# Kernel optimization log

Hardware: AMD Instinct MI355X
Metric: run time of the kernel (lower is better)

Reference implementation:

```python
import jax, jax.numpy as jnp
import numpy as np

B = 8
S = 512  # seq_len


def setup_inputs() -> dict:
    key = jax.random.key(0)
    kx, kw, kb = jax.random.split(key, 3)
    x = jax.random.normal(kx, (B, S, S), dtype=jnp.float32)
    # Padded block of per-diagonal Linear weights: W[i, k, j] is weight[k, j]
    # of nn.Linear(i+1, i+1); entries with k > i or j > i are zero.
    i_d = jnp.arange(S)[:, None, None]
    k_d = jnp.arange(S)[None, :, None]
    j_d = jnp.arange(S)[None, None, :]
    wmask = ((k_d <= i_d) & (j_d <= i_d)).astype(jnp.float32)
    W = jax.random.normal(kw, (S, S, S), dtype=jnp.float32) * 0.02 * wmask
    bmask = (jnp.arange(S)[None, :] <= jnp.arange(S)[:, None]).astype(jnp.float32)
    b = jax.random.normal(kb, (S, S), dtype=jnp.float32) * 0.02 * bmask
    return {"x": x, "W": W, "b": b}


def reference(x, W, b):
    # For each anti-diagonal i (positions (r, i-r), r=0..i, with r+c=i<S):
    #   gather d = x[:, r, i-r], apply Linear_i: out = d @ W_i^T + b_i,
    #   scatter back reversed: x[:, r, i-r] = out[i-r]  =>  x[b,r,c]=out[b,r+c,c].
    S_ = x.shape[-1]
    i_idx = jnp.arange(S_)[:, None]   # diagonal index
    r_idx = jnp.arange(S_)[None, :]   # position along diagonal
    cols = (i_idx - r_idx) % S_
    valid = (r_idx <= i_idx)[None]                       # [1,S,S]
    # D[b, i, r] = x[b, r, i-r] for r<=i else 0
    D = jnp.where(valid, x[:, r_idx, cols], 0.0)         # [B,S,S]
    # Batched per-diagonal matmul: out[b,i,k] = sum_j W[i,k,j] D[b,i,j] + b[i,k]
    out = jnp.einsum('bij,ikj->bik', D, W) + b[None]     # [B,S,S]
    # Scatter back with reversal: x[b,r,c] = out[b, r+c, c] when r+c < S
    rr = jnp.arange(S_)[:, None]
    cc = jnp.arange(S_)[None, :]
    diag = rr + cc
    ok = (diag < S_)[None]
    new_x = jnp.where(ok, out[:, jnp.minimum(diag, S_ - 1), cc], x)
    return new_x
```

## Files before the change

kernel.cpp:

```cpp
#include <hip/hip_runtime.h>

#define S 512
#define NB 8
#define KT 256
#define JT 32

__global__ __launch_bounds__(256) void tail_copy_kernel(const float* __restrict__ x,
                                                        float* __restrict__ out) {
  int idx = blockIdx.x * 256 + threadIdx.x;
  int c = idx & (S - 1);
  int r = (idx >> 9) & (S - 1);
  if (r + c >= S) out[idx] = x[idx];
}

__global__ __launch_bounds__(256, 3) void diag_linear_kernel(const float* __restrict__ x,
                                                             const float* __restrict__ W,
                                                             const float* __restrict__ bias,
                                                             float* __restrict__ out) {
  __shared__ __align__(16) float WtBuf[JT * KT];
  __shared__ __align__(16) float DlBuf[S * NB];

  const int bx = (int)blockIdx.x;
  const int u  = bx >> 3;
  const int xc = bx & 7;
  const int i  = (S - 1) - ((u & 15) + 16 * (xc + 8 * (u >> 4)));
  const int k0 = (int)blockIdx.y * KT;
  if (k0 > i) return;

  const int tid  = threadIdx.x;
  const int wave = tid >> 6;
  const int lane = tid & 63;

  const int jend = (i + JT) & ~(JT - 1);
  const int T    = jend >> 5;

  for (int idx = tid; idx < jend * NB; idx += 256) {
    const int j = idx >> 3;
    const int b = idx & 7;
    DlBuf[idx] = (j <= i) ? x[b * (S * S) + j * S + (i - j)] : 0.0f;
  }

  float acc[4][NB];
#pragma unroll
  for (int m = 0; m < 4; ++m)
#pragma unroll
    for (int b = 0; b < NB; ++b) acc[m][b] = 0.0f;

  const int  k       = k0 + tid;
  const bool krow_ok = (k <= i);
  const float* wrow  = W + ((size_t)i * S + k) * S;

  float4 v[2][8];
  if (!krow_ok) {
#pragma unroll
    for (int g = 0; g < 2; ++g)
#pragma unroll
      for (int q = 0; q < 8; ++q) v[g][q] = make_float4(0.f, 0.f, 0.f, 0.f);
  }

#define LOAD_GRP(g, J0)                                                        \
  if (krow_ok) {                                                               \
    _Pragma("unroll")                                                          \
    for (int q = 0; q < 8; ++q)                                                \
      v[g][q] = *(const float4*)(wrow + (J0) + 4 * q);                         \
  }

  LOAD_GRP(0, 0)
  if (T > 1) LOAD_GRP(1, 32)

  for (int t = 0; t < T; ++t) {
    const int pb = t & 1;
    const int j0 = t << 5;
    __syncthreads();
    {
      const float4* vv = v[pb];
#pragma unroll
      for (int q = 0; q < 8; ++q) {
        WtBuf[(4 * q + 0) * KT + tid] = vv[q].x;
        WtBuf[(4 * q + 1) * KT + tid] = vv[q].y;
        WtBuf[(4 * q + 2) * KT + tid] = vv[q].z;
        WtBuf[(4 * q + 3) * KT + tid] = vv[q].w;
      }
    }
    const int tn = t + 2;
    if (tn < T) LOAD_GRP(pb, tn << 5)
    __syncthreads();

#pragma unroll
    for (int uu = 0; uu < 8; ++uu) {
      const int jl = (wave << 3) + uu;
      const float4 wv = *(const float4*)&WtBuf[jl * KT + (lane << 2)];
      const float4 dA = *(const float4*)&DlBuf[(j0 + jl) * NB];
      const float4 dB = *(const float4*)&DlBuf[(j0 + jl) * NB + 4];
      const float wm[4] = {wv.x, wv.y, wv.z, wv.w};
#pragma unroll
      for (int m = 0; m < 4; ++m) {
        acc[m][0] = fmaf(wm[m], dA.x, acc[m][0]);
        acc[m][1] = fmaf(wm[m], dA.y, acc[m][1]);
        acc[m][2] = fmaf(wm[m], dA.z, acc[m][2]);
        acc[m][3] = fmaf(wm[m], dA.w, acc[m][3]);
        acc[m][4] = fmaf(wm[m], dB.x, acc[m][4]);
        acc[m][5] = fmaf(wm[m], dB.y, acc[m][5]);
        acc[m][6] = fmaf(wm[m], dB.z, acc[m][6]);
        acc[m][7] = fmaf(wm[m], dB.w, acc[m][7]);
      }
    }
  }

  __syncthreads();
  float* Racc = WtBuf;

  for (int w = 0; w < 4; ++w) {
    if (wave == w) {
#pragma unroll
      for (int b = 0; b < NB; ++b) {
        float4* p = (float4*)&Racc[b * KT + (lane << 2)];
        float4 cur = make_float4(acc[0][b], acc[1][b], acc[2][b], acc[3][b]);
        if (w != 0) {
          float4 old = *p;
          cur.x += old.x; cur.y += old.y; cur.z += old.z; cur.w += old.w;
        }
        *p = cur;
      }
    }
    __syncthreads();
  }

  if (krow_ok) {
    const float bv = bias[i * S + k];
    const int r = i - k;
#pragma unroll
    for (int b = 0; b < NB; ++b)
      out[b * (S * S) + r * S + k] = Racc[b * KT + tid] + bv;
  }
}

extern "C" void kernel_launch(void* const* d_in, const int* in_sizes, int n_in,
                              void* d_out, int out_size, void* d_ws, size_t ws_size,
                              hipStream_t stream) {
  const float* x    = (const float*)d_in[0];
  const float* W    = (const float*)d_in[1];
  const float* bias = (const float*)d_in[2];
  float* out = (float*)d_out;

  (void)d_ws; (void)ws_size; (void)in_sizes; (void)n_in; (void)out_size;

  tail_copy_kernel<<<dim3((NB * S * S) / 256), 256, 0, stream>>>(x, out);
  diag_linear_kernel<<<dim3(S, 2), 256, 0, stream>>>(x, W, bias, out);
}
```

Baseline: 716.9 us.

## Halve k-tile to 128 rows and split j-columns across thread halves

Cuts each block's k-tile from 256 to 128 rows, so the grid grows from 2 to 4 tiles in y. Within a block, the two halves of the threads each load a different 16-column slice of the W row. Each thread now keeps 2 accumulator rows instead of 4, which lowers register pressure and lets the occupancy hint rise to 4 blocks. The intent is more blocks and better load balance across the triangular workload, which matters because this kernel is bandwidth bound on W. The custom block-to-diagonal swizzle is replaced with a plain linear mapping. The cost is that the D gather is repeated by more blocks.

```diff
diff --git a/kernel.cpp b/kernel.cpp
--- a/kernel.cpp
+++ b/kernel.cpp
@@ -2,7 +2,7 @@
 
 #define S 512
 #define NB 8
-#define KT 256
+#define KT 128
 #define JT 32
 
 __global__ __launch_bounds__(256) void tail_copy_kernel(const float* __restrict__ x,
@@ -13,17 +13,14 @@
   if (r + c >= S) out[idx] = x[idx];
 }
 
-__global__ __launch_bounds__(256, 3) void diag_linear_kernel(const float* __restrict__ x,
+__global__ __launch_bounds__(256, 4) void diag_linear_kernel(const float* __restrict__ x,
                                                              const float* __restrict__ W,
                                                              const float* __restrict__ bias,
                                                              float* __restrict__ out) {
   __shared__ __align__(16) float WtBuf[JT * KT];
   __shared__ __align__(16) float DlBuf[S * NB];
 
-  const int bx = (int)blockIdx.x;
-  const int u  = bx >> 3;
-  const int xc = bx & 7;
-  const int i  = (S - 1) - ((u & 15) + 16 * (xc + 8 * (u >> 4)));
+  const int i  = (S - 1) - (int)blockIdx.x;
   const int k0 = (int)blockIdx.y * KT;
   if (k0 > i) return;
 
@@ -40,28 +37,30 @@
     DlBuf[idx] = (j <= i) ? x[b * (S * S) + j * S + (i - j)] : 0.0f;
   }
 
-  float acc[4][NB];
+  const int kl_r = tid & (KT - 1);
+  const int h    = tid >> 7;
+  const int  k_r     = k0 + kl_r;
+  const bool krow_ok = (k_r <= i);
+  const float* wrow  = W + ((size_t)i * S + k_r) * S + (h << 4);
+
+  float acc[2][NB];
 #pragma unroll
-  for (int m = 0; m < 4; ++m)
+  for (int m = 0; m < 2; ++m)
 #pragma unroll
     for (int b = 0; b < NB; ++b) acc[m][b] = 0.0f;
 
-  const int  k       = k0 + tid;
-  const bool krow_ok = (k <= i);
-  const float* wrow  = W + ((size_t)i * S + k) * S;
-
-  float4 v[2][8];
+  float4 v[2][4];
   if (!krow_ok) {
 #pragma unroll
     for (int g = 0; g < 2; ++g)
 #pragma unroll
-      for (int q = 0; q < 8; ++q) v[g][q] = make_float4(0.f, 0.f, 0.f, 0.f);
+      for (int q = 0; q < 4; ++q) v[g][q] = make_float4(0.f, 0.f, 0.f, 0.f);
   }
 
 #define LOAD_GRP(g, J0)                                                        \
   if (krow_ok) {                                                               \
     _Pragma("unroll")                                                          \
-    for (int q = 0; q < 8; ++q)                                                \
+    for (int q = 0; q < 4; ++q)                                                \
       v[g][q] = *(const float4*)(wrow + (J0) + 4 * q);                         \
   }
 
@@ -75,11 +74,12 @@
     {
       const float4* vv = v[pb];
 #pragma unroll
-      for (int q = 0; q < 8; ++q) {
-        WtBuf[(4 * q + 0) * KT + tid] = vv[q].x;
-        WtBuf[(4 * q + 1) * KT + tid] = vv[q].y;
-        WtBuf[(4 * q + 2) * KT + tid] = vv[q].z;
-        WtBuf[(4 * q + 3) * KT + tid] = vv[q].w;
+      for (int q = 0; q < 4; ++q) {
+        const int jl = (h << 4) + (q << 2);
+        WtBuf[(jl + 0) * KT + kl_r] = vv[q].x;
+        WtBuf[(jl + 1) * KT + kl_r] = vv[q].y;
+        WtBuf[(jl + 2) * KT + kl_r] = vv[q].z;
+        WtBuf[(jl + 3) * KT + kl_r] = vv[q].w;
       }
     }
     const int tn = t + 2;
@@ -89,12 +89,12 @@
 #pragma unroll
     for (int uu = 0; uu < 8; ++uu) {
       const int jl = (wave << 3) + uu;
-      const float4 wv = *(const float4*)&WtBuf[jl * KT + (lane << 2)];
+      const float2 wv = *(const float2*)&WtBuf[jl * KT + (lane << 1)];
       const float4 dA = *(const float4*)&DlBuf[(j0 + jl) * NB];
       const float4 dB = *(const float4*)&DlBuf[(j0 + jl) * NB + 4];
-      const float wm[4] = {wv.x, wv.y, wv.z, wv.w};
+      const float wm[2] = {wv.x, wv.y};
 #pragma unroll
-      for (int m = 0; m < 4; ++m) {
+      for (int m = 0; m < 2; ++m) {
         acc[m][0] = fmaf(wm[m], dA.x, acc[m][0]);
         acc[m][1] = fmaf(wm[m], dA.y, acc[m][1]);
         acc[m][2] = fmaf(wm[m], dA.z, acc[m][2]);
@@ -114,11 +114,11 @@
     if (wave == w) {
 #pragma unroll
       for (int b = 0; b < NB; ++b) {
-        float4* p = (float4*)&Racc[b * KT + (lane << 2)];
-        float4 cur = make_float4(acc[0][b], acc[1][b], acc[2][b], acc[3][b]);
+        float2* p = (float2*)&Racc[b * KT + (lane << 1)];
+        float2 cur = make_float2(acc[0][b], acc[1][b]);
         if (w != 0) {
-          float4 old = *p;
-          cur.x += old.x; cur.y += old.y; cur.z += old.z; cur.w += old.w;
+          float2 old = *p;
+          cur.x += old.x; cur.y += old.y;
         }
         *p = cur;
       }
@@ -126,12 +126,17 @@
     __syncthreads();
   }
 
-  if (krow_ok) {
-    const float bv = bias[i * S + k];
-    const int r = i - k;
+  {
+    const int k = k0 + kl_r;
+    if (k <= i) {
+      const float bv = bias[i * S + k];
+      const int r = i - k;
 #pragma unroll
-    for (int b = 0; b < NB; ++b)
-      out[b * (S * S) + r * S + k] = Racc[b * KT + tid] + bv;
+      for (int bq = 0; bq < 4; ++bq) {
+        const int b = (h << 2) + bq;
+        out[b * (S * S) + r * S + k] = Racc[b * KT + kl_r] + bv;
+      }
+    }
   }
 }
 
@@ -146,5 +151,5 @@
   (void)d_ws; (void)ws_size; (void)in_sizes; (void)n_in; (void)out_size;
 
   tail_copy_kernel<<<dim3((NB * S * S) / 256), 256, 0, stream>>>(x, out);
-  diag_linear_kernel<<<dim3(S, 2), 256, 0, stream>>>(x, W, bias, out);
+  diag_linear_kernel<<<dim3(S, S / KT), 256, 0, stream>>>(x, W, bias, out);
 }
```

After: 701.5 us. -2.1%, faster.
